# Kernel optimization log

Measured on AMD Instinct MI355X. Metric: run time of the kernel, lower is better.

The kernel has to match this reference:

```python
import jax, jax.numpy as jnp
import numpy as np

LOG2E = 1.4426950408889634  # 1/ln(2): kernel works in log2 space with exp2


def _mlstm_chunkwise_single(q, k, v, vecI, vecF, chunk_size):
    # q,k: [T,K]; v: [T,V]; vecI,vecF: [T] (log2-space gate preactivations)
    T, K = q.shape
    V = v.shape[-1]
    BT = chunk_size
    NT = T // BT
    scale = K ** -0.5
    dt = q.dtype

    qc = q.reshape(NT, BT, K)
    kc = k.reshape(NT, BT, K)
    vc = v.reshape(NT, BT, V)
    ic = vecI.reshape(NT, BT)
    fc = vecF.reshape(NT, BT)
    b = jnp.cumsum(fc, axis=1)            # within-chunk cumulative log2 forget (vecF in kernel)
    f_last = b[:, -1]                      # scaF_last
    g = ic + f_last[:, None] - b           # decay from each pos to chunk end (vecG)

    tri = jnp.tril(jnp.ones((BT, BT), dtype=bool))

    def step(carry, inp):
        C, n, m = carry                    # [K,V], [K], scalar running max
        qt, kt, vt, it, bt, gt, fl = inp
        # intra-chunk decay matrix D[t,s] = i[s] + b[t] - b[s] for s<=t
        D = it[None, :] + bt[:, None] - bt[None, :]
        D = jnp.where(tri, D, -jnp.inf)
        m_intra = jnp.max(D, axis=1)                      # [BT]
        m_total = jnp.maximum(bt + m, m_intra)            # matM_total
        S = (qt @ kt.T) * (scale * jnp.exp2(D - m_total[:, None]))
        q_sc = qt * (scale * jnp.exp2(bt + m - m_total))[:, None]
        h_num = q_sc @ C + S @ vt                          # [BT,V]
        denom = jnp.maximum(jnp.abs(q_sc @ n + S.sum(axis=1)), jnp.exp2(-m_total))
        h = h_num / denom[:, None]
        # cross-chunk matrix-state recurrence with log2 restabilization
        m_next = jnp.maximum(fl + m, jnp.max(gt))
        dec = jnp.exp2(fl + m - m_next)
        kdec = kt * jnp.exp2(gt - m_next)[:, None]         # [BT,K]
        C_next = C * dec + kdec.T @ vt
        n_next = n * dec + kdec.sum(axis=0)
        return (C_next, n_next, m_next), h

    C0 = jnp.zeros((K, V), dt)
    n0 = jnp.zeros((K,), dt)
    m0 = jnp.zeros((), dt)
    _, hs = jax.lax.scan(step, (C0, n0, m0), (qc, kc, vc, ic, b, g, f_last))
    return hs.reshape(T, V)


def setup_inputs() -> dict:
    key = jax.random.key(0)
    ks = jax.random.split(key, 5)
    B, H, T, D = 8, 8, 4096, 64
    q = jax.random.normal(ks[0], (B, H, T, D), dtype=jnp.float32)
    k = jax.random.normal(ks[1], (B, H, T, D), dtype=jnp.float32)
    v = jax.random.normal(ks[2], (B, H, T, D), dtype=jnp.float32)
    i = jax.random.normal(ks[3], (B, H, T), dtype=jnp.float32)
    f = jax.random.normal(ks[4], (B, H, T), dtype=jnp.float32)
    return {"q": q, "k": k, "v": v, "i": i, "f": f, "chunk_size": 64}


def reference(q, k, v, i, f, chunk_size):
    B, H, T, K = q.shape
    V = v.shape[-1]
    vecF = jax.nn.log_sigmoid(f) * LOG2E   # log2 sigmoid(f)
    vecI = i * LOG2E                       # input gate in log2 space
    BH = B * H
    fn = lambda qq, kk, vv, ii, ff: _mlstm_chunkwise_single(qq, kk, vv, ii, ff, chunk_size)
    h = jax.vmap(fn)(q.reshape(BH, T, K), k.reshape(BH, T, K), v.reshape(BH, T, V),
                     vecI.reshape(BH, T), vecF.reshape(BH, T))
    return h.reshape(B, H, T, V)
```

## Files before the change

kernel.cpp:

```cpp
#include <hip/hip_runtime.h>
#include <hip/hip_bf16.h>
#include <math.h>

#define LOG2E_F 1.4426950408889634f

static constexpr int BT = 64;
static constexpr int DK = 64;
static constexpr int DV = 64;
static constexpr float SCALE = 0.125f;
static constexpr int PAD = 72;

typedef unsigned short ushort_t;
typedef __attribute__((ext_vector_type(8))) short short8;
typedef __attribute__((ext_vector_type(4))) float f32x4;
typedef __attribute__((ext_vector_type(4))) ushort_t ushort4v;

#define MFMA16(a, b, c) __builtin_amdgcn_mfma_f32_16x16x32_bf16((a), (b), (c), 0, 0, 0)

__device__ __forceinline__ int SWZ(int a, int b){ return a * PAD + (b ^ (((a >> 3) & 3) << 3)); }
__device__ __forceinline__ int ZSW(int r, int c){ return r * PAD + (c ^ (((r >> 2) & 3) << 3)); }
__device__ __forceinline__ int LIN(int r, int c){ return r * PAD + c; }

__device__ __forceinline__ float logsig_log2e(float x){
    float l = (x >= 0.f) ? (-log1pf(expf(-x))) : (x - log1pf(expf(x)));
    return l * LOG2E_F;
}
__device__ __forceinline__ ushort_t f2bf(float x){
    unsigned u = __builtin_bit_cast(unsigned, x);
    unsigned r = u + 0x7FFFu + ((u >> 16) & 1u);
    return (ushort_t)(r >> 16);
}
__device__ __forceinline__ float bf2f(ushort_t u){
    return __builtin_bit_cast(float, ((unsigned)u) << 16);
}
__device__ __forceinline__ void split_bf(float x, ushort_t& h, ushort_t& l){
    h = f2bf(x);
    l = f2bf(x - bf2f(h));
}

__global__ __launch_bounds__(256, 4) void stageA_kernel(
    const float* __restrict__ kg, const float* __restrict__ vg,
    const float* __restrict__ ig, const float* __restrict__ fg,
    float* __restrict__ A_ws, float* __restrict__ nloc_ws,
    float* __restrict__ fl_ws, float* __restrict__ mloc_ws,
    int T, int NT)
{
    const int ct = blockIdx.x, s = blockIdx.y, tid = threadIdx.x;
    const int w = tid >> 6, lane = tid & 63, ln = lane & 15, quad = lane >> 4;
    const int q8 = quad * 8;

    __shared__ __align__(16) ushort_t kth[BT * PAD];
    __shared__ __align__(16) ushort_t ktl[BT * PAD];
    __shared__ __align__(16) ushort_t vth[BT * PAD];
    __shared__ __align__(16) ushort_t vtl[BT * PAD];
    __shared__ float gsc[BT];

    const size_t rowbase = (size_t)s * T + (size_t)ct * BT;
    const float* kc = kg + rowbase * DK;
    const float* vc = vg + rowbase * DV;

    float4 kr[4], vr[4];
    #pragma unroll
    for (int i = 0; i < 4; ++i){
        int idx = i * 1024 + tid * 4;
        kr[i] = *(const float4*)(kc + idx);
        vr[i] = *(const float4*)(vc + idx);
    }
    if (tid < 64){
        float b = logsig_log2e(fg[rowbase + tid]);
        #pragma unroll
        for (int off = 1; off < 64; off <<= 1){
            float y = __shfl_up(b, off);
            if (tid >= off) b += y;
        }
        float f_last = __shfl(b, 63);
        float a = ig[rowbase + tid] * LOG2E_F - b;
        float p = a;
        #pragma unroll
        for (int off = 32; off > 0; off >>= 1) p = fmaxf(p, __shfl_xor(p, off));
        gsc[tid] = exp2f(a - p);
        if (tid == 0){ fl_ws[s * NT + ct] = f_last; mloc_ws[s * NT + ct] = f_last + p; }
    }
    __syncthreads();
    #pragma unroll
    for (int i = 0; i < 4; ++i){
        int idx = i * 1024 + tid * 4;
        int r = idx >> 6, c0 = idx & 63;
        float g = gsc[r];
        float kv[4] = {kr[i].x * g, kr[i].y * g, kr[i].z * g, kr[i].w * g};
        float vv[4] = {vr[i].x, vr[i].y, vr[i].z, vr[i].w};
        #pragma unroll
        for (int j = 0; j < 4; ++j){
            ushort_t h, l;
            split_bf(kv[j], h, l); kth[SWZ(c0 + j, r)] = h; ktl[SWZ(c0 + j, r)] = l;
            split_bf(vv[j], h, l); vth[SWZ(c0 + j, r)] = h; vtl[SWZ(c0 + j, r)] = l;
        }
    }
    __syncthreads();

    const int m = 16 * w + ln;
    short8 ah0 = *(const short8*)&kth[SWZ(m, q8)];
    short8 ah1 = *(const short8*)&kth[SWZ(m, 32 + q8)];
    short8 al0 = *(const short8*)&ktl[SWZ(m, q8)];
    short8 al1 = *(const short8*)&ktl[SWZ(m, 32 + q8)];
    float* Ab = A_ws + (size_t)(s * NT + ct) * 4096;
    #pragma unroll
    for (int t = 0; t < 4; ++t){
        f32x4 acc = {0.f, 0.f, 0.f, 0.f};
        short8 bh0 = *(const short8*)&vth[SWZ(16 * t + ln, q8)];
        short8 bh1 = *(const short8*)&vth[SWZ(16 * t + ln, 32 + q8)];
        short8 bl0 = *(const short8*)&vtl[SWZ(16 * t + ln, q8)];
        short8 bl1 = *(const short8*)&vtl[SWZ(16 * t + ln, 32 + q8)];
        acc = MFMA16(ah0, bh0, acc);
        acc = MFMA16(ah1, bh1, acc);
        acc = MFMA16(ah0, bl0, acc);
        acc = MFMA16(ah1, bl1, acc);
        acc = MFMA16(al0, bh0, acc);
        acc = MFMA16(al1, bh1, acc);
        #pragma unroll
        for (int reg = 0; reg < 4; ++reg){
            int row = 16 * w + quad * 4 + reg;
            Ab[t * 1024 + row * 16 + ln] = acc[reg];
        }
    }
    {
        short8 ones;
        #pragma unroll
        for (int j = 0; j < 8; ++j) ones[j] = (short)0x3F80;
        f32x4 nacc = {0.f, 0.f, 0.f, 0.f};
        nacc = MFMA16(ah0, ones, nacc);
        nacc = MFMA16(ah1, ones, nacc);
        nacc = MFMA16(al0, ones, nacc);
        nacc = MFMA16(al1, ones, nacc);
        if (ln == 0){
            #pragma unroll
            for (int reg = 0; reg < 4; ++reg)
                nloc_ws[((size_t)(s * NT + ct)) * DK + 16 * w + quad * 4 + reg] = nacc[reg];
        }
    }
}

__global__ __launch_bounds__(256) void stageB_kernel(
    const float* __restrict__ A_ws, const float* __restrict__ nloc_ws,
    const float* __restrict__ fl_ws, const float* __restrict__ mloc_ws,
    float* __restrict__ Cws, float* __restrict__ nws, float* __restrict__ mws,
    int NT)
{
    const int vb = blockIdx.x, s = blockIdx.y, tid = threadIdx.x;
    __shared__ float decs[64], scs[64];

    if (tid < 64){
        float fl = fl_ws[s * NT + tid];
        float ml = mloc_ws[s * NT + tid];
        float F = fl, G = ml;
        #pragma unroll
        for (int off = 1; off < 64; off <<= 1){
            float Fp = __shfl_up(F, off);
            float Gp = __shfl_up(G, off);
            if (tid >= off){ G = fmaxf(Gp + F, G); F = Fp + F; }
        }
        float m_next = fmaxf(F, G);
        float m_cur  = __shfl_up(m_next, 1);
        if (tid == 0) m_cur = 0.f;
        decs[tid] = exp2f(fl + m_cur - m_next);
        scs[tid]  = exp2f(ml - m_next);
        if (vb == 0) mws[s * NT + tid] = m_cur;
    }
    __syncthreads();

    const size_t base = (size_t)s * NT * 4096 + (size_t)vb * 256 + tid;
    const float* Ab = A_ws + base;
    float*       Cb = Cws  + base;
    const bool do_n = (vb == 0) && (tid < 64);

    float C = 0.f, nreg = 0.f;
    float p[8], nl[8];
    #pragma unroll
    for (int i = 0; i < 8; ++i){ p[i] = Ab[(size_t)i * 4096]; nl[i] = 0.f; }
    if (do_n){
        #pragma unroll
        for (int i = 0; i < 8; ++i) nl[i] = nloc_ws[((size_t)(s * NT + i)) * DK + tid];
    }

    for (int t0 = 0; t0 < NT; t0 += 8){
        float qv[8], nq[8];
        const int tn = t0 + 8;
        #pragma unroll
        for (int i = 0; i < 8; ++i)
            qv[i] = (tn + i < NT) ? Ab[(size_t)(tn + i) * 4096] : 0.f;
        #pragma unroll
        for (int i = 0; i < 8; ++i) nq[i] = 0.f;
        if (do_n){
            #pragma unroll
            for (int i = 0; i < 8; ++i)
                if (tn + i < NT) nq[i] = nloc_ws[((size_t)(s * NT + tn + i)) * DK + tid];
        }
        #pragma unroll
        for (int i = 0; i < 8; ++i){
            const int t = t0 + i;
            Cb[(size_t)t * 4096] = C;
            if (do_n) nws[((size_t)(s * NT + t)) * DK + tid] = nreg;
            const float d = decs[t], sc = scs[t];
            C = C * d + p[i] * sc;
            if (do_n) nreg = nreg * d + nl[i] * sc;
        }
        #pragma unroll
        for (int i = 0; i < 8; ++i){ p[i] = qv[i]; nl[i] = nq[i]; }
    }
}

__global__ __launch_bounds__(256, 4) void pass2_kernel(
    const float* __restrict__ qg, const float* __restrict__ kg, const float* __restrict__ vg,
    const float* __restrict__ ig, const float* __restrict__ fg,
    const float* __restrict__ Cws, const float* __restrict__ nws, const float* __restrict__ mws,
    float* __restrict__ out, int T, int NT)
{
    const int ct = blockIdx.x, s = blockIdx.y, tid = threadIdx.x;
    const int w = tid >> 6, lane = tid & 63, ln = lane & 15, quad = lane >> 4;
    const int q8 = quad * 8;

    __shared__ __align__(16) ushort_t bufA[BT * PAD];
    __shared__ __align__(16) ushort_t bufB[BT * PAD];
    __shared__ __align__(16) ushort_t bufC[BT * PAD];
    __shared__ __align__(16) ushort_t bufD[BT * PAD];
    __shared__ float colterm[BT], Mr[BT], rowfac[BT], dncl[BT];
    __shared__ float nsh[DK], qn[BT], rowsum[BT];

    const size_t rowbase = (size_t)s * T + (size_t)ct * BT;
    const float* qc = qg + rowbase * DK;
    const float* kc = kg + rowbase * DK;
    const float* vc = vg + rowbase * DV;
    const float* Cc = Cws + ((size_t)(s * NT + ct)) * 4096;
    const float* nc = nws + ((size_t)(s * NT + ct)) * DK;
    const float m   = mws[s * NT + ct];

    float4 qr[4], kr4[4], vr[4], Cr[4];
    #pragma unroll
    for (int i = 0; i < 4; ++i){
        int idx = i * 1024 + tid * 4;
        qr[i]  = *(const float4*)(qc + idx);
        kr4[i] = *(const float4*)(kc + idx);
        vr[i]  = *(const float4*)(vc + idx);
        Cr[i]  = *(const float4*)(Cc + idx);
    }
    if (tid < 64){
        float b = logsig_log2e(fg[rowbase + tid]);
        #pragma unroll
        for (int off = 1; off < 64; off <<= 1){
            float y = __shfl_up(b, off);
            if (tid >= off) b += y;
        }
        float a = ig[rowbase + tid] * LOG2E_F - b;
        float p = a;
        #pragma unroll
        for (int off = 1; off < 64; off <<= 1){
            float y = __shfl_up(p, off);
            if (tid >= off) p = fmaxf(p, y);
        }
        float M = fmaxf(m, p);
        colterm[tid] = a;
        Mr[tid] = M;
        rowfac[tid] = SCALE * exp2f(m - M);
        dncl[tid] = exp2f(-(b + M));
        nsh[tid] = nc[tid];
    }
    #pragma unroll
    for (int i = 0; i < 4; ++i){
        int idx = i * 1024 + tid * 4;
        int r = idx >> 6, c0 = idx & 63;
        float qv[4] = {qr[i].x, qr[i].y, qr[i].z, qr[i].w};
        float kv[4] = {kr4[i].x, kr4[i].y, kr4[i].z, kr4[i].w};
        ushort4v qh4, ql4, kh4, kl4;
        #pragma unroll
        for (int j = 0; j < 4; ++j){
            ushort_t h, l;
            split_bf(qv[j], h, l); qh4[j] = h; ql4[j] = l;
            split_bf(kv[j], h, l); kh4[j] = h; kl4[j] = l;
        }
        *(ushort4v*)&bufA[LIN(r, c0)] = qh4;
        *(ushort4v*)&bufB[LIN(r, c0)] = ql4;
        *(ushort4v*)&bufC[SWZ(r, c0)] = kh4;
        *(ushort4v*)&bufD[SWZ(r, c0)] = kl4;
    }
    __syncthreads();

    const int mrow = 16 * w + ln;
    short8 ah0 = *(const short8*)&bufA[LIN(mrow, q8)];
    short8 ah1 = *(const short8*)&bufA[LIN(mrow, 32 + q8)];
    short8 al0 = *(const short8*)&bufB[LIN(mrow, q8)];
    short8 al1 = *(const short8*)&bufB[LIN(mrow, 32 + q8)];

    {
        float p = 0.f;
        #pragma unroll
        for (int j = 0; j < 8; ++j){
            float qv0 = bf2f((ushort_t)ah0[j]) + bf2f((ushort_t)al0[j]);
            float qv1 = bf2f((ushort_t)ah1[j]) + bf2f((ushort_t)al1[j]);
            p = fmaf(qv0, nsh[q8 + j], p);
            p = fmaf(qv1, nsh[32 + q8 + j], p);
        }
        p += __shfl_xor(p, 16);
        p += __shfl_xor(p, 32);
        if (quad == 0) qn[mrow] = p;
    }
    __syncthreads();

    #pragma unroll
    for (int i = 0; i < 4; ++i){
        int idx = i * 1024 + tid * 4;
        int r = idx >> 6, c0 = idx & 63;
        float vv[4] = {vr[i].x, vr[i].y, vr[i].z, vr[i].w};
        #pragma unroll
        for (int j = 0; j < 4; ++j) bufB[SWZ(c0 + j, r)] = f2bf(vv[j]);
    }

    f32x4 sacc[4];
    #pragma unroll
    for (int t = 0; t < 4; ++t){
        sacc[t] = (f32x4){0.f, 0.f, 0.f, 0.f};
        short8 bh0 = *(const short8*)&bufC[SWZ(16 * t + ln, q8)];
        short8 bh1 = *(const short8*)&bufC[SWZ(16 * t + ln, 32 + q8)];
        short8 bl0 = *(const short8*)&bufD[SWZ(16 * t + ln, q8)];
        short8 bl1 = *(const short8*)&bufD[SWZ(16 * t + ln, 32 + q8)];
        sacc[t] = MFMA16(ah0, bh0, sacc[t]);
        sacc[t] = MFMA16(ah1, bh1, sacc[t]);
        sacc[t] = MFMA16(ah0, bl0, sacc[t]);
        sacc[t] = MFMA16(ah1, bl1, sacc[t]);
        sacc[t] = MFMA16(al0, bh0, sacc[t]);
        sacc[t] = MFMA16(al1, bh1, sacc[t]);
    }
    {
        float rsum[4] = {0.f, 0.f, 0.f, 0.f};
        float Mrv[4];
        #pragma unroll
        for (int reg = 0; reg < 4; ++reg) Mrv[reg] = Mr[16 * w + quad * 4 + reg];
        #pragma unroll
        for (int t = 0; t < 4; ++t){
            int c = 16 * t + ln;
            float cterm = colterm[c];
            #pragma unroll
            for (int reg = 0; reg < 4; ++reg){
                int r = 16 * w + quad * 4 + reg;
                float vS = (c <= r) ? sacc[t][reg] * SCALE * exp2f(cterm - Mrv[reg]) : 0.f;
                bufA[ZSW(r, c)] = f2bf(vS);
                rsum[reg] += vS;
            }
        }
        #pragma unroll
        for (int off = 1; off < 16; off <<= 1){
            #pragma unroll
            for (int reg = 0; reg < 4; ++reg) rsum[reg] += __shfl_xor(rsum[reg], off);
        }
        if (ln == 0){
            #pragma unroll
            for (int reg = 0; reg < 4; ++reg) rowsum[16 * w + quad * 4 + reg] = rsum[reg];
        }
    }
    __syncthreads();

    #pragma unroll
    for (int i = 0; i < 4; ++i){
        int idx = i * 1024 + tid * 4;
        int vsl = idx >> 10, krow = (idx >> 4) & 63, ci = idx & 15;
        int v0 = vsl * 16 + ci;
        float cv[4] = {Cr[i].x, Cr[i].y, Cr[i].z, Cr[i].w};
        #pragma unroll
        for (int j = 0; j < 4; ++j){
            ushort_t h, l;
            split_bf(cv[j], h, l);
            bufC[SWZ(v0 + j, krow)] = h;
            bufD[SWZ(v0 + j, krow)] = l;
        }
    }
    __syncthreads();

    f32x4 acc[4];
    #pragma unroll
    for (int t = 0; t < 4; ++t){
        acc[t] = (f32x4){0.f, 0.f, 0.f, 0.f};
        short8 bh0 = *(const short8*)&bufC[SWZ(16 * t + ln, q8)];
        short8 bh1 = *(const short8*)&bufC[SWZ(16 * t + ln, 32 + q8)];
        short8 bl0 = *(const short8*)&bufD[SWZ(16 * t + ln, q8)];
        short8 bl1 = *(const short8*)&bufD[SWZ(16 * t + ln, 32 + q8)];
        acc[t] = MFMA16(ah0, bh0, acc[t]);
        acc[t] = MFMA16(ah1, bh1, acc[t]);
        acc[t] = MFMA16(ah0, bl0, acc[t]);
        acc[t] = MFMA16(ah1, bl1, acc[t]);
        acc[t] = MFMA16(al0, bh0, acc[t]);
        acc[t] = MFMA16(al1, bh1, acc[t]);
    }
    float rf[4], inv[4];
    #pragma unroll
    for (int reg = 0; reg < 4; ++reg){
        int r = 16 * w + quad * 4 + reg;
        rf[reg] = rowfac[r];
        float dn = fabsf(rf[reg] * qn[r] + rowsum[r]);
        inv[reg] = 1.f / fmaxf(dn, dncl[r]);
    }
    #pragma unroll
    for (int t = 0; t < 4; ++t){
        #pragma unroll
        for (int reg = 0; reg < 4; ++reg) acc[t][reg] *= rf[reg];
    }
    short8 az0 = *(const short8*)&bufA[ZSW(mrow, q8)];
    short8 az1 = *(const short8*)&bufA[ZSW(mrow, 32 + q8)];
    #pragma unroll
    for (int t = 0; t < 4; ++t){
        short8 bh0 = *(const short8*)&bufB[SWZ(16 * t + ln, q8)];
        short8 bh1 = *(const short8*)&bufB[SWZ(16 * t + ln, 32 + q8)];
        acc[t] = MFMA16(az0, bh0, acc[t]);
        acc[t] = MFMA16(az1, bh1, acc[t]);
    }
    #pragma unroll
    for (int t = 0; t < 4; ++t){
        int c = 16 * t + ln;
        #pragma unroll
        for (int reg = 0; reg < 4; ++reg){
            int r = 16 * w + quad * 4 + reg;
            out[(rowbase + r) * DV + c] = acc[t][reg] * inv[reg];
        }
    }
}

__global__ __launch_bounds__(256) void fused_kernel(
    const float* __restrict__ qg, const float* __restrict__ kg, const float* __restrict__ vg,
    const float* __restrict__ ig, const float* __restrict__ fg,
    float* __restrict__ out, int T, int NT)
{
    const int s = blockIdx.x;
    const int tid = threadIdx.x;
    const int lane = tid & 63;

    __shared__ float X[BT][DK + 1];
    __shared__ float Y[BT][DK + 1];
    __shared__ float Cb[DK][DV];
    __shared__ __hip_bfloat16 Zh[BT][BT];
    __shared__ float colterm[BT], Mr[BT], rowfac[BT], dncl[BT], gscale[BT];
    __shared__ float nsh[DK], qn[BT], rowsum[BT], denom[BT];
    __shared__ float sh_dec;

    const float* qseq = qg + (size_t)s * T * DK;
    const float* kseq = kg + (size_t)s * T * DK;
    const float* vseq = vg + (size_t)s * T * DV;
    const float* iseq = ig + (size_t)s * T;
    const float* fseq = fg + (size_t)s * T;

    for (int idx = tid; idx < DK * DV; idx += 256) Cb[idx >> 6][idx & 63] = 0.f;
    if (tid < 64) nsh[lane] = 0.f;
    float m = 0.f;
    __syncthreads();

    const int r0 = (tid >> 4) * 4;
    const int c0 = (tid & 15) * 4;
    const int v0 = c0;

    for (int t = 0; t < NT; ++t){
        const size_t rb = (size_t)t * BT;
        if (tid < 64){
            float b = logsig_log2e(fseq[rb + lane]);
            #pragma unroll
            for (int off = 1; off < 64; off <<= 1){
                float y = __shfl_up(b, off);
                if (lane >= off) b += y;
            }
            float f_last = __shfl(b, 63);
            float a = iseq[rb + lane] * LOG2E_F - b;
            float p = a;
            #pragma unroll
            for (int off = 1; off < 64; off <<= 1){
                float y = __shfl_up(p, off);
                if (lane >= off) p = fmaxf(p, y);
            }
            float M = fmaxf(m, p);
            colterm[lane] = a;
            Mr[lane] = M;
            rowfac[lane] = SCALE * exp2f(m - M);
            dncl[lane] = exp2f(-(b + M));
            float g = a + f_last;
            float gm = g;
            #pragma unroll
            for (int off = 32; off > 0; off >>= 1) gm = fmaxf(gm, __shfl_xor(gm, off));
            float m_next = fmaxf(f_last + m, gm);
            gscale[lane] = exp2f(g - m_next);
            if (tid == 0) sh_dec = exp2f(f_last + m - m_next);
            m = m_next;
        }
        #pragma unroll
        for (int base = 0; base < BT * DK; base += 1024){
            int idx = base + tid * 4;
            int r = idx >> 6, c = idx & 63;
            float4 a4 = *(const float4*)(qseq + rb * DK + idx);
            X[r][c] = a4.x; X[r][c+1] = a4.y; X[r][c+2] = a4.z; X[r][c+3] = a4.w;
            float4 b4 = *(const float4*)(kseq + rb * DK + idx);
            Y[r][c] = b4.x; Y[r][c+1] = b4.y; Y[r][c+2] = b4.z; Y[r][c+3] = b4.w;
        }
        __syncthreads();

        float sacc[4][4] = {};
        for (int x = 0; x < DK; ++x){
            float xr[4], yc[4];
            #pragma unroll
            for (int j = 0; j < 4; ++j) xr[j] = X[r0 + j][x];
            #pragma unroll
            for (int j = 0; j < 4; ++j) yc[j] = Y[c0 + j][x];
            #pragma unroll
            for (int j = 0; j < 4; ++j)
                #pragma unroll
                for (int jj = 0; jj < 4; ++jj)
                    sacc[j][jj] = fmaf(xr[j], yc[jj], sacc[j][jj]);
        }
        float rs[4];
        #pragma unroll
        for (int j = 0; j < 4; ++j){
            int r = r0 + j;
            float Mrv = Mr[r];
            float acc = 0.f;
            #pragma unroll
            for (int jj = 0; jj < 4; ++jj){
                int c = c0 + jj;
                float vS = (c <= r) ? sacc[j][jj] * SCALE * exp2f(colterm[c] - Mrv) : 0.f;
                Zh[r][c] = __float2bfloat16(vS);
                acc += vS;
            }
            rs[j] = acc;
        }
        #pragma unroll
        for (int off = 1; off < 16; off <<= 1){
            #pragma unroll
            for (int j = 0; j < 4; ++j) rs[j] += __shfl_xor(rs[j], off);
        }
        if ((tid & 15) == 0){
            #pragma unroll
            for (int j = 0; j < 4; ++j) rowsum[r0 + j] = rs[j];
        }
        float acc1[4][4] = {};
        for (int x = 0; x < DK; ++x){
            float xr[4], yv[4];
            #pragma unroll
            for (int j = 0; j < 4; ++j) xr[j] = X[r0 + j][x];
            #pragma unroll
            for (int j = 0; j < 4; ++j) yv[j] = Cb[x][v0 + j];
            #pragma unroll
            for (int j = 0; j < 4; ++j)
                #pragma unroll
                for (int jj = 0; jj < 4; ++jj)
                    acc1[j][jj] = fmaf(xr[j], yv[jj], acc1[j][jj]);
        }
        if (tid < 64){
            float acc = 0.f;
            for (int x = 0; x < DK; ++x) acc = fmaf(X[lane][x], nsh[x], acc);
            qn[lane] = acc;
        }
        __syncthreads();

        #pragma unroll
        for (int base = 0; base < BT * DV; base += 1024){
            int idx = base + tid * 4;
            int r = idx >> 6, c = idx & 63;
            float4 a4 = *(const float4*)(vseq + rb * DV + idx);
            X[r][c] = a4.x; X[r][c+1] = a4.y; X[r][c+2] = a4.z; X[r][c+3] = a4.w;
        }
        if (tid < 64){
            float dn = fabsf(rowfac[lane] * qn[lane] + rowsum[lane]);
            denom[lane] = fmaxf(dn, dncl[lane]);
        }
        __syncthreads();

        float acc2[4][4] = {};
        for (int c = 0; c < BT; ++c){
            float zr[4], xv[4];
            #pragma unroll
            for (int j = 0; j < 4; ++j) zr[j] = __bfloat162float(Zh[r0 + j][c]);
            #pragma unroll
            for (int j = 0; j < 4; ++j) xv[j] = X[c][v0 + j];
            #pragma unroll
            for (int j = 0; j < 4; ++j)
                #pragma unroll
                for (int jj = 0; jj < 4; ++jj)
                    acc2[j][jj] = fmaf(zr[j], xv[jj], acc2[j][jj]);
        }
        #pragma unroll
        for (int j = 0; j < 4; ++j){
            int r = r0 + j;
            float rf = rowfac[r];
            float inv = 1.f / denom[r];
            float4 h4;
            h4.x = (acc1[j][0] * rf + acc2[j][0]) * inv;
            h4.y = (acc1[j][1] * rf + acc2[j][1]) * inv;
            h4.z = (acc1[j][2] * rf + acc2[j][2]) * inv;
            h4.w = (acc1[j][3] * rf + acc2[j][3]) * inv;
            *(float4*)(out + ((size_t)s * T + rb + r) * DV + v0) = h4;
        }
        {
            float dec = sh_dec;
            float cr[4][4];
            #pragma unroll
            for (int j = 0; j < 4; ++j)
                #pragma unroll
                for (int jj = 0; jj < 4; ++jj)
                    cr[j][jj] = Cb[r0 + j][c0 + jj] * dec;
            for (int c = 0; c < BT; ++c){
                float gs = gscale[c];
                float kd[4], xv[4];
                #pragma unroll
                for (int j = 0; j < 4; ++j) kd[j] = Y[c][r0 + j] * gs;
                #pragma unroll
                for (int jj = 0; jj < 4; ++jj) xv[jj] = X[c][c0 + jj];
                #pragma unroll
                for (int j = 0; j < 4; ++j)
                    #pragma unroll
                    for (int jj = 0; jj < 4; ++jj)
                        cr[j][jj] = fmaf(kd[j], xv[jj], cr[j][jj]);
            }
            #pragma unroll
            for (int j = 0; j < 4; ++j)
                #pragma unroll
                for (int jj = 0; jj < 4; ++jj)
                    Cb[r0 + j][c0 + jj] = cr[j][jj];
        }
        if (tid < 64){
            float acc = 0.f;
            for (int c = 0; c < BT; ++c) acc = fmaf(Y[c][lane], gscale[c], acc);
            nsh[lane] = nsh[lane] * sh_dec + acc;
        }
        __syncthreads();
    }
}

extern "C" void kernel_launch(void* const* d_in, const int* in_sizes, int n_in,
                              void* d_out, int out_size, void* d_ws, size_t ws_size,
                              hipStream_t stream)
{
    const float* q  = (const float*)d_in[0];
    const float* k  = (const float*)d_in[1];
    const float* v  = (const float*)d_in[2];
    const float* ii = (const float*)d_in[3];
    const float* ff = (const float*)d_in[4];
    float* out = (float*)d_out;

    const int T  = 4096;
    const int BH = in_sizes[3] / T;
    const int NT = T / BT;

    const size_t szC  = (size_t)BH * NT * DK * DV * sizeof(float);
    const size_t szA  = szC;
    const size_t szn  = (size_t)BH * NT * DK * sizeof(float);
    const size_t szs  = (size_t)BH * NT * sizeof(float);

    const size_t need_new = szA + szC + 2 * szn + 3 * szs;

    if (ws_size >= need_new){
        char* p = (char*)d_ws;
        float* A_ws    = (float*)p;            p += szA;
        float* Cws     = (float*)p;            p += szC;
        float* nloc_ws = (float*)p;            p += szn;
        float* nws     = (float*)p;            p += szn;
        float* fl_ws   = (float*)p;            p += szs;
        float* mloc_ws = (float*)p;            p += szs;
        float* mws     = (float*)p;
        stageA_kernel<<<dim3(NT, BH), 256, 0, stream>>>(k, v, ii, ff, A_ws, nloc_ws, fl_ws, mloc_ws, T, NT);
        stageB_kernel<<<dim3(16, BH), 256, 0, stream>>>(A_ws, nloc_ws, fl_ws, mloc_ws, Cws, nws, mws, NT);
        pass2_kernel<<<dim3(NT, BH), 256, 0, stream>>>(q, k, v, ii, ff, Cws, nws, mws, out, T, NT);
    } else {
        fused_kernel<<<dim3(BH), 256, 0, stream>>>(q, k, v, ii, ff, out, T, NT);
    }
}
```

Baseline: 292.4 us.

## Load Q fragments directly to registers and store C state transposed for vectorized writes

The chunk-state kernel now writes each MFMA accumulator as one 16-byte vector store in a transposed (V-major) layout instead of four scalar strided stores. Pass2 reads Q straight from global memory into MFMA operand registers, which removes the Q staging in LDS and one barrier. Because C is now stored transposed, it can be split and written to LDS with vector stores instead of scattered scalar ones. LDS buffers are renamed and reused, which keeps the footprint the same but means the cross-kernel workspace layout must stay consistent between the two kernels.

```diff
diff --git a/kernel.cpp b/kernel.cpp
--- a/kernel.cpp
+++ b/kernel.cpp
@@ -117,11 +117,7 @@
         acc = MFMA16(ah1, bl1, acc);
         acc = MFMA16(al0, bh0, acc);
         acc = MFMA16(al1, bh1, acc);
-        #pragma unroll
-        for (int reg = 0; reg < 4; ++reg){
-            int row = 16 * w + quad * 4 + reg;
-            Ab[t * 1024 + row * 16 + ln] = acc[reg];
-        }
+        *(f32x4*)(Ab + ((16 * t + ln) << 6) + 16 * w + quad * 4) = acc;
     }
     {
         short8 ones;
@@ -221,8 +217,8 @@
 
     __shared__ __align__(16) ushort_t bufA[BT * PAD];
     __shared__ __align__(16) ushort_t bufB[BT * PAD];
-    __shared__ __align__(16) ushort_t bufC[BT * PAD];
-    __shared__ __align__(16) ushort_t bufD[BT * PAD];
+    __shared__ __align__(16) ushort_t bufZ[BT * PAD];
+    __shared__ __align__(16) ushort_t bufV[BT * PAD];
     __shared__ float colterm[BT], Mr[BT], rowfac[BT], dncl[BT];
     __shared__ float nsh[DK], qn[BT], rowsum[BT];
 
@@ -234,15 +230,23 @@
     const float* nc = nws + ((size_t)(s * NT + ct)) * DK;
     const float m   = mws[s * NT + ct];
 
-    float4 qr[4], kr4[4], vr[4], Cr[4];
+    float4 kr4[4], vr[4];
     #pragma unroll
     for (int i = 0; i < 4; ++i){
         int idx = i * 1024 + tid * 4;
-        qr[i]  = *(const float4*)(qc + idx);
         kr4[i] = *(const float4*)(kc + idx);
         vr[i]  = *(const float4*)(vc + idx);
-        Cr[i]  = *(const float4*)(Cc + idx);
-    }
+    }
+    const float* qrow = qc + (16 * w + ln) * DK;
+    float4 qf0 = *(const float4*)(qrow + q8);
+    float4 qf1 = *(const float4*)(qrow + q8 + 4);
+    float4 qf2 = *(const float4*)(qrow + 32 + q8);
+    float4 qf3 = *(const float4*)(qrow + 32 + q8 + 4);
+    float4 Cr[4];
+    #pragma unroll
+    for (int i = 0; i < 4; ++i)
+        Cr[i] = *(const float4*)(Cc + i * 1024 + tid * 4);
+
     if (tid < 64){
         float b = logsig_log2e(fg[rowbase + tid]);
         #pragma unroll
@@ -268,60 +272,56 @@
     for (int i = 0; i < 4; ++i){
         int idx = i * 1024 + tid * 4;
         int r = idx >> 6, c0 = idx & 63;
-        float qv[4] = {qr[i].x, qr[i].y, qr[i].z, qr[i].w};
         float kv[4] = {kr4[i].x, kr4[i].y, kr4[i].z, kr4[i].w};
-        ushort4v qh4, ql4, kh4, kl4;
+        ushort4v kh4, kl4;
         #pragma unroll
         for (int j = 0; j < 4; ++j){
             ushort_t h, l;
-            split_bf(qv[j], h, l); qh4[j] = h; ql4[j] = l;
             split_bf(kv[j], h, l); kh4[j] = h; kl4[j] = l;
         }
-        *(ushort4v*)&bufA[LIN(r, c0)] = qh4;
-        *(ushort4v*)&bufB[LIN(r, c0)] = ql4;
-        *(ushort4v*)&bufC[SWZ(r, c0)] = kh4;
-        *(ushort4v*)&bufD[SWZ(r, c0)] = kl4;
+        *(ushort4v*)&bufA[SWZ(r, c0)] = kh4;
+        *(ushort4v*)&bufB[SWZ(r, c0)] = kl4;
     }
     __syncthreads();
 
     const int mrow = 16 * w + ln;
-    short8 ah0 = *(const short8*)&bufA[LIN(mrow, q8)];
-    short8 ah1 = *(const short8*)&bufA[LIN(mrow, 32 + q8)];
-    short8 al0 = *(const short8*)&bufB[LIN(mrow, q8)];
-    short8 al1 = *(const short8*)&bufB[LIN(mrow, 32 + q8)];
-
+    float a0[8] = {qf0.x, qf0.y, qf0.z, qf0.w, qf1.x, qf1.y, qf1.z, qf1.w};
+    float a1[8] = {qf2.x, qf2.y, qf2.z, qf2.w, qf3.x, qf3.y, qf3.z, qf3.w};
+    short8 ah0, al0, ah1, al1;
+    #pragma unroll
+    for (int j = 0; j < 8; ++j){
+        ushort_t h, l;
+        split_bf(a0[j], h, l); ah0[j] = (short)h; al0[j] = (short)l;
+        split_bf(a1[j], h, l); ah1[j] = (short)h; al1[j] = (short)l;
+    }
     {
         float p = 0.f;
         #pragma unroll
         for (int j = 0; j < 8; ++j){
-            float qv0 = bf2f((ushort_t)ah0[j]) + bf2f((ushort_t)al0[j]);
-            float qv1 = bf2f((ushort_t)ah1[j]) + bf2f((ushort_t)al1[j]);
-            p = fmaf(qv0, nsh[q8 + j], p);
-            p = fmaf(qv1, nsh[32 + q8 + j], p);
+            p = fmaf(a0[j], nsh[q8 + j], p);
+            p = fmaf(a1[j], nsh[32 + q8 + j], p);
         }
         p += __shfl_xor(p, 16);
         p += __shfl_xor(p, 32);
         if (quad == 0) qn[mrow] = p;
     }
-    __syncthreads();
-
     #pragma unroll
     for (int i = 0; i < 4; ++i){
         int idx = i * 1024 + tid * 4;
         int r = idx >> 6, c0 = idx & 63;
         float vv[4] = {vr[i].x, vr[i].y, vr[i].z, vr[i].w};
         #pragma unroll
-        for (int j = 0; j < 4; ++j) bufB[SWZ(c0 + j, r)] = f2bf(vv[j]);
+        for (int j = 0; j < 4; ++j) bufV[SWZ(c0 + j, r)] = f2bf(vv[j]);
     }
 
     f32x4 sacc[4];
     #pragma unroll
     for (int t = 0; t < 4; ++t){
         sacc[t] = (f32x4){0.f, 0.f, 0.f, 0.f};
-        short8 bh0 = *(const short8*)&bufC[SWZ(16 * t + ln, q8)];
-        short8 bh1 = *(const short8*)&bufC[SWZ(16 * t + ln, 32 + q8)];
-        short8 bl0 = *(const short8*)&bufD[SWZ(16 * t + ln, q8)];
-        short8 bl1 = *(const short8*)&bufD[SWZ(16 * t + ln, 32 + q8)];
+        short8 bh0 = *(const short8*)&bufA[SWZ(16 * t + ln, q8)];
+        short8 bh1 = *(const short8*)&bufA[SWZ(16 * t + ln, 32 + q8)];
+        short8 bl0 = *(const short8*)&bufB[SWZ(16 * t + ln, q8)];
+        short8 bl1 = *(const short8*)&bufB[SWZ(16 * t + ln, 32 + q8)];
         sacc[t] = MFMA16(ah0, bh0, sacc[t]);
         sacc[t] = MFMA16(ah1, bh1, sacc[t]);
         sacc[t] = MFMA16(ah0, bl0, sacc[t]);
@@ -342,7 +342,7 @@
             for (int reg = 0; reg < 4; ++reg){
                 int r = 16 * w + quad * 4 + reg;
                 float vS = (c <= r) ? sacc[t][reg] * SCALE * exp2f(cterm - Mrv[reg]) : 0.f;
-                bufA[ZSW(r, c)] = f2bf(vS);
+                bufZ[ZSW(r, c)] = f2bf(vS);
                 rsum[reg] += vS;
             }
         }
@@ -361,16 +361,16 @@
     #pragma unroll
     for (int i = 0; i < 4; ++i){
         int idx = i * 1024 + tid * 4;
-        int vsl = idx >> 10, krow = (idx >> 4) & 63, ci = idx & 15;
-        int v0 = vsl * 16 + ci;
+        int vrow = idx >> 6, k0 = idx & 63;
         float cv[4] = {Cr[i].x, Cr[i].y, Cr[i].z, Cr[i].w};
+        ushort4v ch4, cl4;
         #pragma unroll
         for (int j = 0; j < 4; ++j){
             ushort_t h, l;
-            split_bf(cv[j], h, l);
-            bufC[SWZ(v0 + j, krow)] = h;
-            bufD[SWZ(v0 + j, krow)] = l;
-        }
+            split_bf(cv[j], h, l); ch4[j] = h; cl4[j] = l;
+        }
+        *(ushort4v*)&bufA[SWZ(vrow, k0)] = ch4;
+        *(ushort4v*)&bufB[SWZ(vrow, k0)] = cl4;
     }
     __syncthreads();
 
@@ -378,10 +378,10 @@
     #pragma unroll
     for (int t = 0; t < 4; ++t){
         acc[t] = (f32x4){0.f, 0.f, 0.f, 0.f};
-        short8 bh0 = *(const short8*)&bufC[SWZ(16 * t + ln, q8)];
-        short8 bh1 = *(const short8*)&bufC[SWZ(16 * t + ln, 32 + q8)];
-        short8 bl0 = *(const short8*)&bufD[SWZ(16 * t + ln, q8)];
-        short8 bl1 = *(const short8*)&bufD[SWZ(16 * t + ln, 32 + q8)];
+        short8 bh0 = *(const short8*)&bufA[SWZ(16 * t + ln, q8)];
+        short8 bh1 = *(const short8*)&bufA[SWZ(16 * t + ln, 32 + q8)];
+        short8 bl0 = *(const short8*)&bufB[SWZ(16 * t + ln, q8)];
+        short8 bl1 = *(const short8*)&bufB[SWZ(16 * t + ln, 32 + q8)];
         acc[t] = MFMA16(ah0, bh0, acc[t]);
         acc[t] = MFMA16(ah1, bh1, acc[t]);
         acc[t] = MFMA16(ah0, bl0, acc[t]);
@@ -402,12 +402,12 @@
         #pragma unroll
         for (int reg = 0; reg < 4; ++reg) acc[t][reg] *= rf[reg];
     }
-    short8 az0 = *(const short8*)&bufA[ZSW(mrow, q8)];
-    short8 az1 = *(const short8*)&bufA[ZSW(mrow, 32 + q8)];
+    short8 az0 = *(const short8*)&bufZ[ZSW(mrow, q8)];
+    short8 az1 = *(const short8*)&bufZ[ZSW(mrow, 32 + q8)];
     #pragma unroll
     for (int t = 0; t < 4; ++t){
-        short8 bh0 = *(const short8*)&bufB[SWZ(16 * t + ln, q8)];
-        short8 bh1 = *(const short8*)&bufB[SWZ(16 * t + ln, 32 + q8)];
+        short8 bh0 = *(const short8*)&bufV[SWZ(16 * t + ln, q8)];
+        short8 bh1 = *(const short8*)&bufV[SWZ(16 * t + ln, 32 + q8)];
         acc[t] = MFMA16(az0, bh0, acc[t]);
         acc[t] = MFMA16(az1, bh1, acc[t]);
     }
```

Result: no change. 292.1 us (-0.1%).
